# Kernel optimization log

Measured on AMD Instinct MI355X. Metric: run time of the kernel, lower is better.

The kernel has to match this reference:

```python
import jax, jax.numpy as jnp
import numpy as np

B, T, C, H = 64, 256, 384, 6
HS = C // H  # 64
EPS = 1e-3  # keras LayerNormalization default epsilon


def layernorm(x, gamma, beta):
    mu = jnp.mean(x, axis=-1, keepdims=True)
    var = jnp.var(x, axis=-1, keepdims=True)
    return (x - mu) * jax.lax.rsqrt(var + EPS) * gamma + beta


def setup_inputs() -> dict:
    key = jax.random.key(0)
    ks = jax.random.split(key, 12)
    s = lambda fan_in: 1.0 / np.sqrt(fan_in)
    return {
        "x": jax.random.normal(ks[0], (B, T, C), dtype=jnp.float32),
        "Wq": jax.random.normal(ks[1], (H, C, HS), dtype=jnp.float32) * s(C),
        "Wk": jax.random.normal(ks[2], (H, C, HS), dtype=jnp.float32) * s(C),
        "Wv": jax.random.normal(ks[3], (H, C, HS), dtype=jnp.float32) * s(C),
        "Wp": jax.random.normal(ks[4], (C, C), dtype=jnp.float32) * s(C),
        "bp": jnp.zeros((C,), dtype=jnp.float32),
        "W1": jax.random.normal(ks[5], (C, 4 * C), dtype=jnp.float32) * s(C),
        "b1": jnp.zeros((4 * C,), dtype=jnp.float32),
        "W2": jax.random.normal(ks[6], (4 * C, C), dtype=jnp.float32) * s(4 * C),
        "b2": jnp.zeros((C,), dtype=jnp.float32),
        "g1": jnp.ones((C,), dtype=jnp.float32),
        "be1": jnp.zeros((C,), dtype=jnp.float32),
        "g2": jnp.ones((C,), dtype=jnp.float32),
        "be2": jnp.zeros((C,), dtype=jnp.float32),
    }


def reference(x, Wq, Wk, Wv, Wp, bp, W1, b1, W2, b2, g1, be1, g2, be2):
    # --- self-attention sub-block (dropout is identity at inference) ---
    h = layernorm(x, g1, be1)                              # [B,T,C]
    q = jnp.einsum('btc,hcd->bhtd', h, Wq)                 # [B,H,T,HS]
    k = jnp.einsum('btc,hcd->bhtd', h, Wk)
    v = jnp.einsum('btc,hcd->bhtd', h, Wv)
    scale = HS ** -0.5
    wei = jnp.einsum('bhtd,bhsd->bhts', q, k) * scale      # [B,H,T,T]
    causal = jnp.tril(jnp.ones((T, T), dtype=bool))
    wei = jnp.where(causal[None, None], wei, -jnp.inf)
    att = jax.nn.softmax(wei, axis=-1)
    o = jnp.einsum('bhts,bhsd->bthd', att, v).reshape(B, T, C)  # concat heads
    sa = o @ Wp + bp
    x = x + sa
    # --- feed-forward sub-block ---
    h2 = layernorm(x, g2, be2)
    ff = jax.nn.relu(h2 @ W1 + b1) @ W2 + b2
    return x + ff
```

## Files before the change

### kernel.cpp

```cpp
#include <hip/hip_runtime.h>
#include <hip/hip_bf16.h>
#include <math.h>

#define Bn 64
#define Tn 256
#define Cn 384
#define Hn 6
#define HSn 64
#define FFn 1536
#define EPSn 1e-3f
#define SECn 6291456

typedef __attribute__((ext_vector_type(4))) float f32x4;
typedef __attribute__((ext_vector_type(2))) float f32x2;
typedef __attribute__((ext_vector_type(8))) short short8;
typedef __attribute__((ext_vector_type(4))) short short4v;
typedef __attribute__((ext_vector_type(2))) short short2v;

__device__ __forceinline__ void async_copy16(void* lds, const void* g) {
    __builtin_amdgcn_global_load_lds(
        (const __attribute__((address_space(1))) void*)g,
        (__attribute__((address_space(3))) void*)lds, 16, 0, 0);
}

__device__ __forceinline__ short f2bf(float v) {
    __hip_bfloat16 h = __float2bfloat16(v);
    return *(short*)&h;
}


__global__ __launch_bounds__(256) void ln_pack_kernel(const float* __restrict__ x,
                                                      const float* __restrict__ g,
                                                      const float* __restrict__ be,
                                                      __hip_bfloat16* __restrict__ outPk) {
    int mt = blockIdx.x;
    int tid = threadIdx.x;
    int lane = tid & 63, wave = tid >> 6;
    __shared__ short rows[16 * 392];
#pragma unroll
    for (int i = 0; i < 4; i++) {
        int r = wave * 4 + i;
        const float* xr = x + ((size_t)mt * 16 + r) * Cn;
        f32x4 a = *(const f32x4*)(xr + lane * 4);
        f32x2 b = *(const f32x2*)(xr + 256 + lane * 2);
        float s = a.x + a.y + a.z + a.w + b.x + b.y;
#pragma unroll
        for (int off = 32; off; off >>= 1) s += __shfl_xor(s, off);
        float mu = s * (1.0f / Cn);
        f32x4 da = a - mu;
        f32x2 db = b - mu;
        float sq = da.x * da.x + da.y * da.y + da.z * da.z + da.w * da.w + db.x * db.x + db.y * db.y;
#pragma unroll
        for (int off = 32; off; off >>= 1) sq += __shfl_xor(sq, off);
        float rs = rsqrtf(sq * (1.0f / Cn) + EPSn);
        f32x4 g4 = *(const f32x4*)(g + lane * 4);
        f32x2 g2 = *(const f32x2*)(g + 256 + lane * 2);
        f32x4 e4 = *(const f32x4*)(be + lane * 4);
        f32x2 e2 = *(const f32x2*)(be + 256 + lane * 2);
        f32x4 y4 = da * rs * g4 + e4;
        f32x2 y2 = db * rs * g2 + e2;
        short4v o4 = {f2bf(y4.x), f2bf(y4.y), f2bf(y4.z), f2bf(y4.w)};
        *(short4v*)(&rows[r * 392 + lane * 4]) = o4;
        short2v o2 = {f2bf(y2.x), f2bf(y2.y)};
        *(short2v*)(&rows[r * 392 + 256 + lane * 2]) = o2;
    }
    __syncthreads();
    int r = lane & 15, q = lane >> 4;
#pragma unroll
    for (int p = 0; p < 3; p++) {
        int f = p * 4 + (tid >> 6);
        short8 v = *(const short8*)(&rows[r * 392 + f * 32 + q * 8]);
        *(short8*)((short*)outPk + ((size_t)mt * 12 + f) * 512 + lane * 8) = v;
    }
}

__global__ __launch_bounds__(256) void pack_b_kernel(const float* __restrict__ W,
                                                     __hip_bfloat16* __restrict__ out,
                                                     int K, int N) {
    int id = blockIdx.x * 256 + threadIdx.x;
    if (id >= K * N) return;
    int tile = id >> 9, lane = (id >> 3) & 63, j = id & 7;
    int ntiles = N >> 4;
    int k = (tile / ntiles) * 32 + ((lane >> 4) << 3) + j;
    int n = (tile % ntiles) * 16 + (lane & 15);
    out[id] = __float2bfloat16(W[(size_t)k * N + n]);
}

__global__ __launch_bounds__(256) void pack_qkv_kernel(const float* __restrict__ Wq,
                                                       const float* __restrict__ Wk,
                                                       const float* __restrict__ Wv,
                                                       __hip_bfloat16* __restrict__ out) {
    int id = blockIdx.x * 256 + threadIdx.x;
    if (id >= Cn * 1152) return;
    int tile = id >> 9, lane = (id >> 3) & 63, j = id & 7;
    int k = (tile / 72) * 32 + ((lane >> 4) << 3) + j;
    int n = (tile % 72) * 16 + (lane & 15);
    int sec = n / Cn, rem = n % Cn;
    int hh = rem >> 6, d = rem & 63;
    const float* W = (sec == 0) ? Wq : ((sec == 1) ? Wk : Wv);
    out[id] = __float2bfloat16(W[((size_t)hh * Cn + k) * HSn + d]);
}

template <int KK, int NN, int EPI>
__global__ __launch_bounds__(256) void gemm_mfma(const __hip_bfloat16* __restrict__ Apk,
                                                 const __hip_bfloat16* __restrict__ Bp,
                                                 const float* __restrict__ bias,
                                                 const float* __restrict__ resid,
                                                 float* __restrict__ outF,
                                                 __hip_bfloat16* __restrict__ outB) {
    constexpr int GX = NN / 64;
    constexpr int K32 = KK / 32;
    constexpr int NC = K32 / 4;
    constexpr int NT16 = NN / 16;
    __shared__ __align__(16) short ldsB[2 * 8192];

    int l = blockIdx.x;
    int xcd = l & 7, i = l >> 3;
    int rowblk = xcd * 16 + i / GX;
    int colblk = i - (i / GX) * GX;

    int lane = threadIdx.x & 63, wave = threadIdx.x >> 6;
    int lrow = lane & 15, lquad = lane >> 4;
    int m0 = rowblk * 128;
    int n0 = colblk * 64;
    int mt0 = (m0 >> 4) + wave * 2;

    f32x4 acc[2][4];
#pragma unroll
    for (int st = 0; st < 2; st++)
#pragma unroll
        for (int nt = 0; nt < 4; nt++) acc[st][nt] = (f32x4){0.f, 0.f, 0.f, 0.f};

    const short* a0p = (const short*)Apk + ((size_t)mt0 * K32) * 512 + lane * 8;
    const short* a1p = a0p + (size_t)K32 * 512;
    const short* bsrc = (const short*)Bp + ((size_t)wave * NT16 + (n0 >> 4)) * 512 + lane * 8;
    short* bdst0 = ldsB + wave * 2048;

#pragma unroll
    for (int nt = 0; nt < 4; nt++) async_copy16(bdst0 + nt * 512, bsrc + nt * 512);
    short8 aR[2][2][4];
#pragma unroll
    for (int kf = 0; kf < 4; kf++) {
        aR[0][0][kf] = *(const short8*)(a0p + kf * 512);
        aR[0][1][kf] = *(const short8*)(a1p + kf * 512);
    }

#pragma unroll
    for (int c = 0; c < NC; c++) {
        __syncthreads();
        if (c + 1 < NC) {
            const short* bs = bsrc + (size_t)(c + 1) * 4 * NT16 * 512;
            short* bd = ldsB + ((c + 1) & 1) * 8192 + wave * 2048;
#pragma unroll
            for (int nt = 0; nt < 4; nt++) async_copy16(bd + nt * 512, bs + nt * 512);
#pragma unroll
            for (int kf = 0; kf < 4; kf++) {
                aR[(c + 1) & 1][0][kf] = *(const short8*)(a0p + ((c + 1) * 4 + kf) * 512);
                aR[(c + 1) & 1][1][kf] = *(const short8*)(a1p + ((c + 1) * 4 + kf) * 512);
            }
        }
        const short* bl = ldsB + (c & 1) * 8192 + lane * 8;
#pragma unroll
        for (int kf = 0; kf < 4; kf++) {
#pragma unroll
            for (int nt = 0; nt < 4; nt++) {
                short8 bf = *(const short8*)(bl + (kf * 4 + nt) * 512);
                acc[0][nt] = __builtin_amdgcn_mfma_f32_16x16x32_bf16(aR[c & 1][0][kf], bf,
                                                                     acc[0][nt], 0, 0, 0);
                acc[1][nt] = __builtin_amdgcn_mfma_f32_16x16x32_bf16(aR[c & 1][1][kf], bf,
                                                                     acc[1][nt], 0, 0, 0);
            }
        }
    }
    __syncthreads();

    if (EPI == 1) {
        float* twf = (float*)((char*)ldsB + wave * 4864);
        float bnv[4];
#pragma unroll
        for (int nt = 0; nt < 4; nt++) bnv[nt] = bias[n0 + nt * 16 + lrow];
#pragma unroll
        for (int st = 0; st < 2; st++) {
            int mbase = m0 + (2 * wave + st) * 16;
#pragma unroll
            for (int nt = 0; nt < 4; nt++)
#pragma unroll
                for (int r = 0; r < 4; r++)
                    twf[(lquad * 4 + r) * 76 + nt * 16 + lrow] = acc[st][nt][r] + bnv[nt];
            int row = lane >> 2, seg = lane & 3;
            int m = mbase + row;
            const float* rrow = resid + (size_t)m * NN + n0 + seg * 16;
            float* orow = outF + (size_t)m * NN + n0 + seg * 16;
#pragma unroll
            for (int c = 0; c < 4; c++) {
                f32x4 vv = *(const f32x4*)(&twf[row * 76 + seg * 16 + c * 4]);
                f32x4 rv = *(const f32x4*)(rrow + c * 4);
                *(f32x4*)(orow + c * 4) = vv + rv;
            }
            __builtin_amdgcn_s_waitcnt(0);
        }
    } else {
        short* tws = (short*)((char*)ldsB + wave * 4864);
        float bnv[4];
        if (EPI == 2) {
#pragma unroll
            for (int nt = 0; nt < 4; nt++) bnv[nt] = bias[n0 + nt * 16 + lrow];
        }
#pragma unroll
        for (int st = 0; st < 2; st++)
#pragma unroll
            for (int nt = 0; nt < 4; nt++)
#pragma unroll
                for (int r = 0; r < 4; r++) {
                    float v = acc[st][nt][r];
                    if (EPI == 2) v = fmaxf(v + bnv[nt], 0.0f);
                    tws[(st * 16 + lquad * 4 + r) * 72 + nt * 16 + lrow] = f2bf(v);
                }
        if (EPI == 2) {
#pragma unroll
            for (int st2 = 0; st2 < 2; st2++) {
                int mt = (m0 >> 4) + wave * 2 + st2;
#pragma unroll
                for (int kcl = 0; kcl < 2; kcl++) {
                    int kc = (n0 >> 5) + kcl;
                    short8 v = *(const short8*)(
                        &tws[(st2 * 16 + (lane & 15)) * 72 + kcl * 32 + (lane >> 4) * 8]);
                    *(short8*)((short*)outB + ((size_t)mt * (NN / 32) + kc) * 512 + lane * 8) = v;
                }
            }
        } else {
            int sec = n0 / 384;
            int rem0 = n0 - sec * 384;
            int hh = rem0 >> 6;
            int b = m0 >> 8;
            int t_base = (m0 & 255) + wave * 32;
            int bh2 = b * Hn + hh;
            if (sec < 2) {
                short* outp = (short*)outB + (size_t)sec * SECn + (size_t)bh2 * 16384 +
                              (size_t)(t_base >> 4) * 1024 + lane * 8;
#pragma unroll
                for (int st2 = 0; st2 < 2; st2++)
#pragma unroll
                    for (int kc = 0; kc < 2; kc++) {
                        short8 v8 = *(const short8*)(
                            &tws[(st2 * 16 + (lane & 15)) * 72 + kc * 32 + (lane >> 4) * 8]);
                        *(short8*)(outp + (st2 * 2 + kc) * 512) = v8;
                    }
            } else {
                short* vout = (short*)outB + (size_t)2 * SECn + (size_t)bh2 * 16384 +
                              (size_t)((t_base >> 5) * 4) * 512;
#pragma unroll
                for (int dt = 0; dt < 4; dt++) {
                    short8 v8;
#pragma unroll
                    for (int j = 0; j < 8; j++) {
                        int t_loc = ((lane >> 4) << 3) + j;
                        v8[j] = tws[t_loc * 72 + dt * 16 + (lane & 15)];
                    }
                    *(short8*)(vout + dt * 512 + lane * 8) = v8;
                }
            }
        }
    }
}

__global__ __launch_bounds__(256) void attn_mfma_kernel(const __hip_bfloat16* __restrict__ qp,
                                                        const __hip_bfloat16* __restrict__ kp,
                                                        const __hip_bfloat16* __restrict__ vp,
                                                        __hip_bfloat16* __restrict__ o) {
    __shared__ short Pl[4 * 4096];
    int blk = blockIdx.x;
    int bh = blk % (Bn * Hn);
    int jg = blk / (Bn * Hn);
    int b = bh / Hn, hh = bh - b * Hn;
    int tid = threadIdx.x;
    int lane = tid & 63, wave = tid >> 6;
    int c16 = lane & 15, quad = lane >> 4;
    int qt = (wave << 2) + ((wave & 1) ? (3 - jg) : jg);

    const short* qs = (const short*)qp + (size_t)bh * 16384 + (size_t)qt * 1024 + lane * 8;
    const short* ks = (const short*)kp + (size_t)bh * 16384 + lane * 8;
    const short* vs = (const short*)vp + (size_t)bh * 16384 + lane * 8;
    short* Pw = Pl + wave * 4096;

    short8 aq0 = *(const short8*)(qs);
    short8 aq1 = *(const short8*)(qs + 512);

    int st_max = qt;
    int kb_count = (qt + 2) >> 1;
    int covered = kb_count * 2;
    int qrow0 = qt * 16;

    f32x4 accS[16];
#pragma unroll
    for (int st = 0; st < 16; st++) accS[st] = (f32x4){0.f, 0.f, 0.f, 0.f};
#pragma unroll
    for (int st = 0; st < 16; st++) {
        if (st <= st_max) {
            short8 bk0 = *(const short8*)(ks + st * 1024);
            short8 bk1 = *(const short8*)(ks + st * 1024 + 512);
            accS[st] = __builtin_amdgcn_mfma_f32_16x16x32_bf16(aq0, bk0, accS[st], 0, 0, 0);
            accS[st] = __builtin_amdgcn_mfma_f32_16x16x32_bf16(aq1, bk1, accS[st], 0, 0, 0);
        }
    }

    float inv[4];
#pragma unroll
    for (int r = 0; r < 4; r++) {
        int row = qrow0 + quad * 4 + r;
        float mx = -INFINITY;
#pragma unroll
        for (int st = 0; st < 16; st++) {
            if (st <= st_max) {
                int col = st * 16 + c16;
                float a = (col <= row) ? accS[st][r] * 0.125f : -INFINITY;
                accS[st][r] = a;
                mx = fmaxf(mx, a);
            }
        }
#pragma unroll
        for (int off = 8; off; off >>= 1) mx = fmaxf(mx, __shfl_xor(mx, off));
        float sum = 0.f;
#pragma unroll
        for (int st = 0; st < 16; st++) {
            if (st < covered) {
                float e = 0.0f;
                if (st <= st_max) {
                    e = __expf(accS[st][r] - mx);
                    sum += e;
                }
                int c = st * 16 + c16;
                Pw[(c >> 5) * 512 + (((c >> 3) & 3) * 16 + quad * 4 + r) * 8 + (c & 7)] =
                    f2bf(e);
            }
        }
#pragma unroll
        for (int off = 8; off; off >>= 1) sum += __shfl_xor(sum, off);
        inv[r] = 1.0f / sum;
    }

    f32x4 accO[4];
#pragma unroll
    for (int nt = 0; nt < 4; nt++) accO[nt] = (f32x4){0.f, 0.f, 0.f, 0.f};
#pragma unroll
    for (int kbi = 0; kbi < 8; kbi++) {
        if (kbi < kb_count) {
            short8 ap = *(const short8*)(Pw + kbi * 512 + lane * 8);
#pragma unroll
            for (int nt = 0; nt < 4; nt++) {
                short8 bv = *(const short8*)(vs + (kbi * 4 + nt) * 512);
                accO[nt] = __builtin_amdgcn_mfma_f32_16x16x32_bf16(ap, bv, accO[nt], 0, 0, 0);
            }
        }
    }

#pragma unroll
    for (int nt = 0; nt < 4; nt++)
#pragma unroll
        for (int r = 0; r < 4; r++)
            Pw[(quad * 4 + r) * 72 + nt * 16 + c16] = f2bf(accO[nt][r] * inv[r]);
    int mt = (b << 4) + qt;
#pragma unroll
    for (int kcl = 0; kcl < 2; kcl++) {
        short8 v = *(const short8*)(&Pw[(lane & 15) * 72 + kcl * 32 + (lane >> 4) * 8]);
        *(short8*)((short*)o + ((size_t)mt * 12 + hh * 2 + kcl) * 512 + lane * 8) = v;
    }
}

extern "C" void kernel_launch(void* const* d_in, const int* in_sizes, int n_in,
                              void* d_out, int out_size, void* d_ws, size_t ws_size,
                              hipStream_t stream) {
    const float* x  = (const float*)d_in[0];
    const float* Wq = (const float*)d_in[1];
    const float* Wk = (const float*)d_in[2];
    const float* Wv = (const float*)d_in[3];
    const float* Wp = (const float*)d_in[4];
    const float* bp = (const float*)d_in[5];
    const float* W1 = (const float*)d_in[6];
    const float* b1 = (const float*)d_in[7];
    const float* W2 = (const float*)d_in[8];
    const float* b2 = (const float*)d_in[9];
    const float* g1 = (const float*)d_in[10];
    const float* be1 = (const float*)d_in[11];
    const float* g2 = (const float*)d_in[12];
    const float* be2 = (const float*)d_in[13];

    const size_t M = (size_t)Bn * Tn;
    __hip_bfloat16* ws  = (__hip_bfloat16*)d_ws;
    __hip_bfloat16* h   = ws;
    __hip_bfloat16* big = h + M * Cn;
    __hip_bfloat16* o   = big + M * FFn;
    __hip_bfloat16* pQKV = o + M * Cn;
    __hip_bfloat16* pWp  = pQKV + Cn * 1152;
    __hip_bfloat16* pW1  = pWp + Cn * Cn;
    __hip_bfloat16* pW2  = pW1 + Cn * FFn;

    float* x2 = (float*)d_out;

    pack_qkv_kernel<<<(Cn * 1152 + 255) / 256, 256, 0, stream>>>(Wq, Wk, Wv, pQKV);
    pack_b_kernel<<<(Cn * Cn + 255) / 256, 256, 0, stream>>>(Wp, pWp, Cn, Cn);
    pack_b_kernel<<<(Cn * FFn + 255) / 256, 256, 0, stream>>>(W1, pW1, Cn, FFn);
    pack_b_kernel<<<(FFn * Cn + 255) / 256, 256, 0, stream>>>(W2, pW2, FFn, Cn);

    ln_pack_kernel<<<M / 16, 256, 0, stream>>>(x, g1, be1, h);
    gemm_mfma<Cn, 1152, 0><<<2304, 256, 0, stream>>>(h, pQKV, nullptr, nullptr, nullptr, big);
    attn_mfma_kernel<<<Bn * Hn * 4, 256, 0, stream>>>(big, big + SECn, big + 2 * SECn, o);
    gemm_mfma<Cn, Cn, 1><<<768, 256, 0, stream>>>(o, pWp, bp, x, x2, nullptr);
    ln_pack_kernel<<<M / 16, 256, 0, stream>>>(x2, g2, be2, h);
    gemm_mfma<Cn, FFn, 2><<<3072, 256, 0, stream>>>(h, pW1, b1, nullptr, nullptr, big);
    gemm_mfma<FFn, Cn, 1><<<768, 256, 0, stream>>>(big, pW2, b2, x2, x2, nullptr);
}
```

Measured before the change: 236.9 us.

## Stage K tiles in shared LDS and process P in two halves

Each block now copies the full K for its batch-head into LDS with async global-to-LDS copies. All four waves then read K from LDS instead of each issuing its own global loads. The probability buffer per wave is halved: softmax exponentials and the PV MFMAs are interleaved over two halves of the key range, and the row-sum reduction is deferred to the end. The cost is a block-wide barrier and more total LDS per block (K plus P), which may reduce occupancy.

```diff
diff --git a/kernel.cpp b/kernel.cpp
--- a/kernel.cpp
+++ b/kernel.cpp
@@ -268,7 +268,8 @@
                                                         const __hip_bfloat16* __restrict__ kp,
                                                         const __hip_bfloat16* __restrict__ vp,
                                                         __hip_bfloat16* __restrict__ o) {
-    __shared__ short Pl[4 * 4096];
+    __shared__ short Kl[16 * 1024];
+    __shared__ short Pl[4 * 2048];
     int blk = blockIdx.x;
     int bh = blk % (Bn * Hn);
     int jg = blk / (Bn * Hn);
@@ -278,10 +279,16 @@
     int c16 = lane & 15, quad = lane >> 4;
     int qt = (wave << 2) + ((wave & 1) ? (3 - jg) : jg);
 
+    const short* ks = (const short*)kp + (size_t)bh * 16384;
+#pragma unroll
+    for (int i = 0; i < 8; i++) {
+        int tile = wave * 8 + i;
+        async_copy16(&Kl[tile * 512], ks + tile * 512 + lane * 8);
+    }
+
     const short* qs = (const short*)qp + (size_t)bh * 16384 + (size_t)qt * 1024 + lane * 8;
-    const short* ks = (const short*)kp + (size_t)bh * 16384 + lane * 8;
     const short* vs = (const short*)vp + (size_t)bh * 16384 + lane * 8;
-    short* Pw = Pl + wave * 4096;
+    short* Pw = Pl + wave * 2048;
 
     short8 aq0 = *(const short8*)(qs);
     short8 aq1 = *(const short8*)(qs + 512);
@@ -291,67 +298,88 @@
     int covered = kb_count * 2;
     int qrow0 = qt * 16;
 
+    __syncthreads();
+
     f32x4 accS[16];
 #pragma unroll
     for (int st = 0; st < 16; st++) accS[st] = (f32x4){0.f, 0.f, 0.f, 0.f};
 #pragma unroll
     for (int st = 0; st < 16; st++) {
         if (st <= st_max) {
-            short8 bk0 = *(const short8*)(ks + st * 1024);
-            short8 bk1 = *(const short8*)(ks + st * 1024 + 512);
+            short8 bk0 = *(const short8*)(&Kl[st * 1024 + lane * 8]);
+            short8 bk1 = *(const short8*)(&Kl[st * 1024 + 512 + lane * 8]);
             accS[st] = __builtin_amdgcn_mfma_f32_16x16x32_bf16(aq0, bk0, accS[st], 0, 0, 0);
             accS[st] = __builtin_amdgcn_mfma_f32_16x16x32_bf16(aq1, bk1, accS[st], 0, 0, 0);
         }
     }
 
-    float inv[4];
+    float mx[4];
 #pragma unroll
     for (int r = 0; r < 4; r++) {
         int row = qrow0 + quad * 4 + r;
-        float mx = -INFINITY;
+        float m = -INFINITY;
 #pragma unroll
         for (int st = 0; st < 16; st++) {
             if (st <= st_max) {
                 int col = st * 16 + c16;
                 float a = (col <= row) ? accS[st][r] * 0.125f : -INFINITY;
                 accS[st][r] = a;
-                mx = fmaxf(mx, a);
-            }
-        }
-#pragma unroll
-        for (int off = 8; off; off >>= 1) mx = fmaxf(mx, __shfl_xor(mx, off));
-        float sum = 0.f;
-#pragma unroll
-        for (int st = 0; st < 16; st++) {
-            if (st < covered) {
-                float e = 0.0f;
-                if (st <= st_max) {
-                    e = __expf(accS[st][r] - mx);
-                    sum += e;
+                m = fmaxf(m, a);
+            }
+        }
+#pragma unroll
+        for (int off = 8; off; off >>= 1) m = fmaxf(m, __shfl_xor(m, off));
+        mx[r] = m;
+    }
+
+    float sum[4] = {0.f, 0.f, 0.f, 0.f};
+    f32x4 accO[4];
+#pragma unroll
+    for (int nt = 0; nt < 4; nt++) accO[nt] = (f32x4){0.f, 0.f, 0.f, 0.f};
+#pragma unroll
+    for (int half = 0; half < 2; half++) {
+        int st_lo = half * 8;
+        if (st_lo < covered) {
+#pragma unroll
+            for (int st2 = 0; st2 < 8; st2++) {
+                int st = st_lo + st2;
+                if (st < covered) {
+#pragma unroll
+                    for (int r = 0; r < 4; r++) {
+                        float e = 0.0f;
+                        if (st <= st_max) {
+                            e = __expf(accS[st][r] - mx[r]);
+                            sum[r] += e;
+                        }
+                        int cl = st2 * 16 + c16;
+                        Pw[(cl >> 5) * 512 + (((cl >> 3) & 3) * 16 + quad * 4 + r) * 8 +
+                           (cl & 7)] = f2bf(e);
+                    }
                 }
-                int c = st * 16 + c16;
-                Pw[(c >> 5) * 512 + (((c >> 3) & 3) * 16 + quad * 4 + r) * 8 + (c & 7)] =
-                    f2bf(e);
-            }
-        }
-#pragma unroll
-        for (int off = 8; off; off >>= 1) sum += __shfl_xor(sum, off);
-        inv[r] = 1.0f / sum;
-    }
-
-    f32x4 accO[4];
-#pragma unroll
-    for (int nt = 0; nt < 4; nt++) accO[nt] = (f32x4){0.f, 0.f, 0.f, 0.f};
-#pragma unroll
-    for (int kbi = 0; kbi < 8; kbi++) {
-        if (kbi < kb_count) {
-            short8 ap = *(const short8*)(Pw + kbi * 512 + lane * 8);
-#pragma unroll
-            for (int nt = 0; nt < 4; nt++) {
-                short8 bv = *(const short8*)(vs + (kbi * 4 + nt) * 512);
-                accO[nt] = __builtin_amdgcn_mfma_f32_16x16x32_bf16(ap, bv, accO[nt], 0, 0, 0);
-            }
-        }
+            }
+#pragma unroll
+            for (int k2 = 0; k2 < 4; k2++) {
+                int kbi = half * 4 + k2;
+                if (kbi < kb_count) {
+                    short8 ap = *(const short8*)(Pw + k2 * 512 + lane * 8);
+#pragma unroll
+                    for (int nt = 0; nt < 4; nt++) {
+                        short8 bv = *(const short8*)(vs + (kbi * 4 + nt) * 512);
+                        accO[nt] = __builtin_amdgcn_mfma_f32_16x16x32_bf16(ap, bv, accO[nt],
+                                                                           0, 0, 0);
+                    }
+                }
+            }
+        }
+    }
+
+    float inv[4];
+#pragma unroll
+    for (int r = 0; r < 4; r++) {
+        float s = sum[r];
+#pragma unroll
+        for (int off = 8; off; off >>= 1) s += __shfl_xor(s, off);
+        inv[r] = 1.0f / s;
     }
 
 #pragma unroll
```

Result: slower. 243.4 us (+2.8%).
